# Optimization experiments

Hardware: AMD Instinct MI355X
Metric: run time of the kernel (lower is better)

Reference implementation:

```python
import jax, jax.numpy as jnp
import numpy as np

DN = ('NCHW', 'OIHW', 'NCHW')
HEADS = 4
EPS_LN = 1e-5
EPS_NORM = 1e-12


def conv(x, w, pad=0, groups=1):
    return jax.lax.conv_general_dilated(
        x, w, window_strides=(1, 1), padding=[(pad, pad), (pad, pad)],
        dimension_numbers=DN, feature_group_count=groups)


def layernorm(x, w, b):
    # LayerNorm over channel axis per spatial position (to_3d -> LN(c) -> to_4d)
    mu = jnp.mean(x, axis=1, keepdims=True)
    var = jnp.mean((x - mu) ** 2, axis=1, keepdims=True)
    return (x - mu) / jnp.sqrt(var + EPS_LN) * w[None, :, None, None] + b[None, :, None, None]


def setup_inputs() -> dict:
    key = jax.random.key(0)
    ks = jax.random.split(key, 12)
    b, dim, h, w = 2, 192, 128, 128
    hidden = int(dim * 2.66)  # 510

    def rn(k, shape, scale=0.05):
        return jax.random.normal(k, shape, dtype=jnp.float32) * scale

    return {
        'x': jax.random.normal(ks[0], (b, dim, h, w), dtype=jnp.float32),
        'illum': jax.random.normal(ks[1], (b, dim, h, w), dtype=jnp.float32),
        'ln1_w': jnp.ones((dim,), jnp.float32), 'ln1_b': jnp.zeros((dim,), jnp.float32),
        'lnL_w': jnp.ones((dim,), jnp.float32), 'lnL_b': jnp.zeros((dim,), jnp.float32),
        'ln2_w': jnp.ones((dim,), jnp.float32), 'ln2_b': jnp.zeros((dim,), jnp.float32),
        'q_w': rn(ks[2], (dim, dim, 1, 1)),
        'qdw_w': rn(ks[3], (dim, dim, 3, 3)),        # full 3x3 conv (no groups in source)
        'kv_w': rn(ks[4], (2 * dim, dim, 1, 1)),
        'kvdw_w': rn(ks[5], (2 * dim, 1, 3, 3)),     # depthwise, groups = 2*dim
        'temp': jnp.ones((HEADS, 1, 1), jnp.float32),
        'proj_w': rn(ks[6], (dim, dim, 1, 1)),
        'pin_w': rn(ks[7], (hidden, dim, 1, 1)),
        'dw_w': rn(ks[8], (hidden, hidden, 3, 3)),   # full 3x3 conv (no groups in source)
        'pout_w': rn(ks[9], (dim, hidden, 1, 1)),
    }


def _block(x, illum, ln1_w, ln1_b, lnL_w, lnL_b, ln2_w, ln2_b,
           q_w, qdw_w, kv_w, kvdw_w, temp, proj_w, pin_w, dw_w, pout_w):
    b, c, h, w = x.shape
    ch = c // HEADS

    # ---- Illum-guided channel attention (MDTA) ----
    xn = layernorm(x, ln1_w, ln1_b)
    iln = layernorm(illum, lnL_w, lnL_b)
    q = conv(conv(iln, q_w), qdw_w, pad=1)
    kv = conv(conv(xn, kv_w), kvdw_w, pad=1, groups=2 * c)
    k, v = jnp.split(kv, 2, axis=1)

    def split_heads(t):
        return t.reshape(b, HEADS, ch, h * w)  # b head c (hw)

    q, k, v = split_heads(q), split_heads(k), split_heads(v)
    q = q / jnp.maximum(jnp.linalg.norm(q, axis=-1, keepdims=True), EPS_NORM)
    k = k / jnp.maximum(jnp.linalg.norm(k, axis=-1, keepdims=True), EPS_NORM)

    attn = jnp.einsum('bhce,bhde->bhcd', q, k) * temp[None]  # [b, head, ch, ch]
    attn = jax.nn.softmax(attn, axis=-1)
    out = jnp.einsum('bhcd,bhde->bhce', attn, v).reshape(b, c, h, w)
    x = x + conv(out, proj_w)

    # ---- FFN: 1x1 -> full 3x3 -> GELU -> 1x1 ----
    xn2 = layernorm(x, ln2_w, ln2_b)
    f = conv(xn2, pin_w)
    f = jax.nn.gelu(conv(f, dw_w, pad=1), approximate=False)
    x = x + conv(f, pout_w)
    return x


def reference(x, illum, ln1_w, ln1_b, lnL_w, lnL_b, ln2_w, ln2_b,
              q_w, qdw_w, kv_w, kvdw_w, temp, proj_w, pin_w, dw_w, pout_w):
    return _block(x, illum, ln1_w, ln1_b, lnL_w, lnL_b, ln2_w, ln2_b,
                  q_w, qdw_w, kv_w, kvdw_w, temp, proj_w, pin_w, dw_w, pout_w)
```

## Files before the change

### kernel.cpp

```cpp
#include <hip/hip_runtime.h>
#include <hip/hip_bf16.h>

typedef __hip_bfloat16 bf16;
typedef __attribute__((ext_vector_type(8))) short bf16x8v;
typedef __attribute__((ext_vector_type(4))) float f32x4;

namespace {
constexpr int B_  = 2;
constexpr int C_  = 192;
constexpr int HW_ = 128 * 128;
constexpr int C2_ = 384;
}

static __device__ __forceinline__ float fb(bf16 v) { return __bfloat162float(v); }
static __device__ __forceinline__ bf16 tob(float v) { return __float2bfloat16(v); }

typedef __attribute__((address_space(1))) const char GChar;
typedef __attribute__((address_space(3))) char LChar;
static __device__ __forceinline__ void gl16(const void* g, void* l) {
    __builtin_amdgcn_global_load_lds((GChar*)g, (LChar*)l, 16, 0, 0);
}
static __device__ __forceinline__ bf16x8v lread(const bf16* base, int row, int slot) {
    const char* p = (const char*)base + (size_t)row * 128 + ((size_t)((slot ^ (row & 7))) << 4);
    return *(const bf16x8v*)p;
}

static __device__ __forceinline__ void rp1(const float* W, bf16* Wr, int blk, int t,
                                           int N, int K, int Npad, int Kpad) {
    int i = blk * 256 + t;
    if (i >= Npad * Kpad) return;
    int n = i / Kpad, k = i % Kpad;
    float v = (n < N && k < K) ? W[n * K + k] : 0.f;
    Wr[i] = tob(v);
}
static __device__ __forceinline__ void rp3(const float* W, bf16* Wr, int blk, int t,
                                           int N, int K, int Npad, int Kpad) {
    int i = blk * 256 + t;
    int NK = Npad * Kpad;
    if (i >= NK) return;
    int n = i / Kpad, k = i % Kpad;
    if (n < N && k < K) {
        const float* src = W + ((size_t)(n * K + k)) * 9;
#pragma unroll
        for (int q = 0; q < 9; q++) Wr[(size_t)q * NK + i] = tob(src[q]);
    } else {
#pragma unroll
        for (int q = 0; q < 9; q++) Wr[(size_t)q * NK + i] = tob(0.f);
    }
}

__global__ __launch_bounds__(256) void k_repack_ln(
    const float* __restrict__ qw, const float* __restrict__ kvw,
    const float* __restrict__ projw, const float* __restrict__ pinw,
    const float* __restrict__ poutw, const float* __restrict__ qdww,
    const float* __restrict__ dww,
    bf16* __restrict__ Wq1, bf16* __restrict__ Wkv, bf16* __restrict__ Wproj,
    bf16* __restrict__ Wpin, bf16* __restrict__ Wpout, bf16* __restrict__ Wqdw,
    bf16* __restrict__ Wdw, char* __restrict__ zpage,
    const float* __restrict__ X0, const float* __restrict__ X1,
    const float* __restrict__ w0, const float* __restrict__ b0,
    const float* __restrict__ w1, const float* __restrict__ b1,
    bf16* __restrict__ out0, bf16* __restrict__ out1) {
    __shared__ float lds[64][C_ + 1];
    int blk = blockIdx.x, t = threadIdx.x;
    if (blk < 144)        { rp1(qw,    Wq1,   blk,        t, 192, 192, 192, 192); return; }
    else if (blk < 432)   { rp1(kvw,   Wkv,   blk - 144,  t, 384, 192, 384, 192); return; }
    else if (blk < 576)   { rp1(projw, Wproj, blk - 432,  t, 192, 192, 192, 192); return; }
    else if (blk < 960)   { rp1(pinw,  Wpin,  blk - 576,  t, 510, 192, 512, 192); return; }
    else if (blk < 1344)  { rp1(poutw, Wpout, blk - 960,  t, 192, 510, 192, 512); return; }
    else if (blk < 1488)  { rp3(qdww,  Wqdw,  blk - 1344, t, 192, 192, 192, 192); return; }
    else if (blk < 2512)  { rp3(dww,   Wdw,   blk - 1488, t, 510, 510, 512, 512); return; }
    else if (blk == 2512) { ((uint4*)zpage)[t] = make_uint4(0u, 0u, 0u, 0u); return; }
    int lb = blk - 2513;
    int sel = lb >> 9, xb = lb & 511;
    const float* X = sel ? X1 : X0;
    const float* w = sel ? w1 : w0;
    const float* bb = sel ? b1 : b0;
    bf16* out = sel ? out1 : out0;
    int p0 = xb * 64;
    int b = p0 / HW_, pi0 = p0 % HW_;
    for (int i = t; i < 64 * C_ / 4; i += 256) {
        int c = i >> 4, pp4 = (i & 15) << 2;
        float4 v = *(const float4*)(X + ((size_t)(b * C_ + c)) * HW_ + pi0 + pp4);
        lds[pp4 + 0][c] = v.x; lds[pp4 + 1][c] = v.y;
        lds[pp4 + 2][c] = v.z; lds[pp4 + 3][c] = v.w;
    }
    __syncthreads();
    int pp = t >> 2, qq = t & 3;
    float s = 0.f, s2 = 0.f;
    for (int c = qq * 48; c < qq * 48 + 48; c++) { float v = lds[pp][c]; s += v; s2 += v * v; }
    s  += __shfl_xor(s, 1);  s  += __shfl_xor(s, 2);
    s2 += __shfl_xor(s2, 1); s2 += __shfl_xor(s2, 2);
    float mu = s / C_;
    float rstd = rsqrtf(s2 / C_ - mu * mu + 1e-5f);
    bf16* ob = out + ((size_t)(p0 + pp)) * C_ + qq * 48;
#pragma unroll
    for (int j = 0; j < 6; j++) {
        union { bf16 h[8]; uint4 u; } ov;
#pragma unroll
        for (int e = 0; e < 8; e++) {
            int c = qq * 48 + j * 8 + e;
            ov.h[e] = tob((lds[pp][c] - mu) * rstd * w[c] + bb[c]);
        }
        *(uint4*)(ob + j * 8) = ov.u;
    }
}

__global__ __launch_bounds__(256) void k_ln_pc(const bf16* __restrict__ X2,
                                               const float* __restrict__ w,
                                               const float* __restrict__ bb,
                                               bf16* __restrict__ out) {
    int t = threadIdx.x;
    int p = blockIdx.x * 64 + (t >> 2), qq = t & 3;
    const bf16* row = X2 + (size_t)p * C_ + qq * 48;
    uint4 u[6];
#pragma unroll
    for (int j = 0; j < 6; j++) u[j] = *(const uint4*)(row + j * 8);
    float s = 0.f, s2 = 0.f;
#pragma unroll
    for (int j = 0; j < 6; j++) {
        const bf16* pv = (const bf16*)&u[j];
#pragma unroll
        for (int e = 0; e < 8; e++) { float v = fb(pv[e]); s += v; s2 += v * v; }
    }
    s  += __shfl_xor(s, 1);  s  += __shfl_xor(s, 2);
    s2 += __shfl_xor(s2, 1); s2 += __shfl_xor(s2, 2);
    float mu = s / C_;
    float rstd = rsqrtf(s2 / C_ - mu * mu + 1e-5f);
    bf16* orow = out + (size_t)p * C_ + qq * 48;
#pragma unroll
    for (int j = 0; j < 6; j++) {
        const bf16* pv = (const bf16*)&u[j];
        union { bf16 h[8]; uint4 u4; } ov;
#pragma unroll
        for (int e = 0; e < 8; e++) {
            int c = qq * 48 + j * 8 + e;
            ov.h[e] = tob((fb(pv[e]) - mu) * rstd * w[c] + bb[c]);
        }
        *(uint4*)(orow + j * 8) = ov.u4;
    }
}

template <int BN, int EPI>
static __device__ __forceinline__ void gemm1x1_body(const bf16* __restrict__ A,
                                                    const bf16* __restrict__ Wbase,
                                                    const int K, const int Cout,
                                                    void* __restrict__ outp,
                                                    const void* __restrict__ resid,
                                                    const int mt, const int n0) {
    constexpr int WN = BN / 2, FN = WN / 16, BIT = BN / 32;
    __shared__ __align__(16) bf16 As[128 * 64];
    __shared__ __align__(16) bf16 Bs[BN * 64];
    const int t = threadIdx.x;
    const int b = mt >> 7, y = mt & 127;
    const int w = t >> 6, lane = t & 63;
    const int wm = w >> 1, wn = w & 1;
    const int g = lane >> 4, r = lane & 15;
    const int ldw = t - lane;

    f32x4 acc[4][FN];
#pragma unroll
    for (int i = 0; i < 4; i++)
#pragma unroll
        for (int j = 0; j < FN; j++) acc[i][j] = {0.f, 0.f, 0.f, 0.f};

    const bf16* Abase = A + (size_t)mt * 128 * K;

    for (int c0 = 0; c0 < K; c0 += 64) {
#pragma unroll
        for (int it = 0; it < 4; it++) {
            int idx = it * 256 + t;
            int row = idx >> 3, sl = idx & 7;
            const char* gp = (const char*)(Abase + (size_t)row * K + c0) + ((sl ^ (row & 7)) << 4);
            gl16(gp, (char*)As + (size_t)(it * 256 + ldw) * 16);
        }
#pragma unroll
        for (int it = 0; it < BIT; it++) {
            int idx = it * 256 + t;
            int row = idx >> 3, sl = idx & 7;
            const char* gp = (const char*)(Wbase + (size_t)(n0 + row) * K + c0) + ((sl ^ (row & 7)) << 4);
            gl16(gp, (char*)Bs + (size_t)(it * 256 + ldw) * 16);
        }
        __syncthreads();
#pragma unroll
        for (int ks = 0; ks < 2; ks++) {
            bf16x8v af[4], bv[FN];
#pragma unroll
            for (int fm = 0; fm < 4; fm++)
                af[fm] = lread(As, wm * 64 + fm * 16 + r, ks * 4 + g);
#pragma unroll
            for (int fn = 0; fn < FN; fn++)
                bv[fn] = lread(Bs, wn * WN + fn * 16 + r, ks * 4 + g);
#pragma unroll
            for (int fm = 0; fm < 4; fm++)
#pragma unroll
                for (int fn = 0; fn < FN; fn++)
                    acc[fm][fn] = __builtin_amdgcn_mfma_f32_16x16x32_bf16(af[fm], bv[fn], acc[fm][fn], 0, 0, 0);
        }
        __syncthreads();
    }

#pragma unroll
    for (int fm = 0; fm < 4; fm++)
#pragma unroll
        for (int fn = 0; fn < FN; fn++)
#pragma unroll
            for (int reg = 0; reg < 4; reg++) {
                int xl = wm * 64 + fm * 16 + g * 4 + reg;
                int co = n0 + wn * WN + fn * 16 + r;
                float v = acc[fm][fn][reg];
                if constexpr (EPI == 1) {
                    ((bf16*)outp)[((size_t)mt * 128 + xl) * Cout + co] = tob(v);
                } else if constexpr (EPI == 2) {
                    v += ((const float*)resid)[((size_t)(b * C_ + co)) * HW_ + y * 128 + xl];
                    ((bf16*)outp)[((size_t)mt * 128 + xl) * C_ + co] = tob(v);
                } else {
                    v += fb(((const bf16*)resid)[((size_t)mt * 128 + xl) * C_ + co]);
                    ((float*)outp)[((size_t)(b * C_ + co)) * HW_ + y * 128 + xl] = v;
                }
            }
}

template <int BN, int EPI>
__global__ __launch_bounds__(256) void k_gemm1x1(const bf16* __restrict__ A,
                                                 const bf16* __restrict__ Wr,
                                                 const int K, const int Cout,
                                                 void* __restrict__ outp,
                                                 const void* __restrict__ resid,
                                                 const int wbstride) {
    const int mt = blockIdx.x;
    const bf16* Wbase = Wr + (size_t)(mt >> 7) * wbstride;
    gemm1x1_body<BN, EPI>(A, Wbase, K, Cout, outp, resid, mt, blockIdx.y * BN);
}

__global__ __launch_bounds__(256) void k_qkv(const bf16* __restrict__ iln,
                                             const bf16* __restrict__ xn,
                                             const bf16* __restrict__ Wq1,
                                             const bf16* __restrict__ Wkv,
                                             bf16* __restrict__ qtmp,
                                             bf16* __restrict__ kvtmp) {
    const bool isq = blockIdx.y < 2;
    const bf16* A = isq ? iln : xn;
    const bf16* Wr = isq ? Wq1 : Wkv;
    bf16* outp = isq ? qtmp : kvtmp;
    const int Cout = isq ? 192 : 384;
    const int n0 = (isq ? blockIdx.y : blockIdx.y - 2) * 96;
    gemm1x1_body<96, 1>(A, Wr, 192, Cout, outp, nullptr, blockIdx.x, n0);
}

template <int BN, int EPI>
__global__ __launch_bounds__(256) void k_gemm3x3(const bf16* __restrict__ A,
                                                 const bf16* __restrict__ Wr,
                                                 const int Cin, const int Cout,
                                                 bf16* __restrict__ outp,
                                                 const char* __restrict__ zpage) {
    constexpr int WN = BN / 2, FN = WN / 16, BIT = BN / 32;
    __shared__ __align__(16) bf16 As[160 * 64];
    __shared__ __align__(16) bf16 Bs[BN * 64];
    const int t = threadIdx.x;
    const int mtRaw = blockIdx.x;
    const int mt = ((mtRaw & 7) << 5) | (mtRaw >> 3);
    const int n0 = blockIdx.y * BN;
    const int b = mt >> 7, y = mt & 127;
    const int w = t >> 6, lane = t & 63;
    const int wm = w >> 1, wn = w & 1;
    const int g = lane >> 4, r = lane & 15;
    const int ldw = t - lane;

    f32x4 acc[4][FN];
#pragma unroll
    for (int i = 0; i < 4; i++)
#pragma unroll
        for (int j = 0; j < FN; j++) acc[i][j] = {0.f, 0.f, 0.f, 0.f};

    for (int ky = 0; ky < 3; ky++) {
        const int yy = y + ky - 1;
        if (yy < 0 || yy > 127) continue;
        const bf16* Ab = A + ((size_t)b * HW_ + (size_t)yy * 128) * Cin;
        for (int c0 = 0; c0 < Cin; c0 += 64) {
            for (int kx = 0; kx < 3; kx++) {
                if (kx == 0) {
#pragma unroll
                    for (int it = 0; it < 5; it++) {
                        int idx = it * 256 + t;
                        int row = idx >> 3, sl = idx & 7;
                        int so = (sl ^ (row & 7)) << 4;
                        const char* gp = (row >= 1 && row <= 128)
                            ? (const char*)(Ab + (size_t)(row - 1) * Cin + c0) + so
                            : zpage + so;
                        gl16(gp, (char*)As + (size_t)(it * 256 + ldw) * 16);
                    }
                }
                const bf16* Wb = Wr + (size_t)(ky * 3 + kx) * Cout * Cin;
#pragma unroll
                for (int it = 0; it < BIT; it++) {
                    int idx = it * 256 + t;
                    int row = idx >> 3, sl = idx & 7;
                    const char* gp = (const char*)(Wb + (size_t)(n0 + row) * Cin + c0) + ((sl ^ (row & 7)) << 4);
                    gl16(gp, (char*)Bs + (size_t)(it * 256 + ldw) * 16);
                }
                __syncthreads();
#pragma unroll
                for (int ks = 0; ks < 2; ks++) {
                    bf16x8v af[4], bv[FN];
#pragma unroll
                    for (int fm = 0; fm < 4; fm++)
                        af[fm] = lread(As, wm * 64 + fm * 16 + r + kx, ks * 4 + g);
#pragma unroll
                    for (int fn = 0; fn < FN; fn++)
                        bv[fn] = lread(Bs, wn * WN + fn * 16 + r, ks * 4 + g);
#pragma unroll
                    for (int fm = 0; fm < 4; fm++)
#pragma unroll
                        for (int fn = 0; fn < FN; fn++)
                            acc[fm][fn] = __builtin_amdgcn_mfma_f32_16x16x32_bf16(af[fm], bv[fn], acc[fm][fn], 0, 0, 0);
                }
                __syncthreads();
            }
        }
    }
#pragma unroll
    for (int fm = 0; fm < 4; fm++)
#pragma unroll
        for (int fn = 0; fn < FN; fn++)
#pragma unroll
            for (int reg = 0; reg < 4; reg++) {
                int xl = wm * 64 + fm * 16 + g * 4 + reg;
                int co = n0 + wn * WN + fn * 16 + r;
                float v = acc[fm][fn][reg];
                if constexpr (EPI == 1) v = 0.5f * v * (1.0f + erff(v * 0.70710678118654752f));
                outp[((size_t)mt * 128 + xl) * Cout + co] = tob(v);
            }
}

__global__ __launch_bounds__(192) void k_dwconv2(const bf16* __restrict__ kv,
                                                 const float* __restrict__ wdw,
                                                 bf16* __restrict__ kout,
                                                 bf16* __restrict__ vout) {
    __shared__ float wlds[1728];
    const int t = threadIdx.x;
    const int row = blockIdx.x;
    const int z = blockIdx.y;
    const int b = row >> 7, y = row & 127;
    for (int i = t; i < 432; i += 192)
        ((float4*)wlds)[i] = ((const float4*)(wdw + (size_t)z * 1728))[i];
    __syncthreads();
    const int c8h = t % 24, xg = t / 24;
    const int cbase = z * C_ + c8h * 8;
    float wreg[9][8];
#pragma unroll
    for (int tap = 0; tap < 9; tap++)
#pragma unroll
        for (int j = 0; j < 8; j++) wreg[tap][j] = wlds[(c8h * 8 + j) * 9 + tap];

    bf16* outb = (z == 0 ? kout : vout) + (size_t)(b * HW_ + y * 128) * C_ + c8h * 8;
    const uint4 zero4 = make_uint4(0u, 0u, 0u, 0u);
    const int x0 = xg * 16;
    bool vy[3]; const bf16* rowp[3];
#pragma unroll
    for (int ky = 0; ky < 3; ky++) {
        int yy = y + ky - 1;
        vy[ky] = (yy >= 0 && yy <= 127);
        int yyc = vy[ky] ? yy : 0;
        rowp[ky] = kv + ((size_t)b * HW_ + (size_t)yyc * 128) * C2_ + cbase;
    }
    uint4 win[3][3];
#pragma unroll
    for (int ky = 0; ky < 3; ky++) {
        win[ky][0] = (vy[ky] && x0 - 1 >= 0) ? *(const uint4*)(rowp[ky] + (size_t)(x0 - 1) * C2_) : zero4;
        win[ky][1] = vy[ky] ? *(const uint4*)(rowp[ky] + (size_t)x0 * C2_) : zero4;
    }
    for (int i = 0; i < 16; i++) {
        int x = x0 + i;
#pragma unroll
        for (int ky = 0; ky < 3; ky++)
            win[ky][2] = (vy[ky] && x + 1 <= 127) ? *(const uint4*)(rowp[ky] + (size_t)(x + 1) * C2_) : zero4;
        float acc[8];
#pragma unroll
        for (int j = 0; j < 8; j++) acc[j] = 0.f;
#pragma unroll
        for (int ky = 0; ky < 3; ky++)
#pragma unroll
            for (int kx = 0; kx < 3; kx++) {
                const bf16* pv = (const bf16*)&win[ky][kx];
#pragma unroll
                for (int j = 0; j < 8; j++)
                    acc[j] += fb(pv[j]) * wreg[ky * 3 + kx][j];
            }
        union { bf16 h[8]; uint4 u; } ov;
#pragma unroll
        for (int j = 0; j < 8; j++) ov.h[j] = tob(acc[j]);
        *(uint4*)(outb + (size_t)x * C_) = ov.u;
#pragma unroll
        for (int ky = 0; ky < 3; ky++) { win[ky][0] = win[ky][1]; win[ky][1] = win[ky][2]; }
    }
}

__global__ __launch_bounds__(256) void k_qk(const bf16* __restrict__ q,
                                            const bf16* __restrict__ k,
                                            float* __restrict__ Spart,
                                            float* __restrict__ ssq) {
    __shared__ float qs[64][49];
    __shared__ float ks[64][49];
    __shared__ float redq[4][48], redk[4][48];
    int t = threadIdx.x;
    int ch = blockIdx.x, hd = blockIdx.y, b = blockIdx.z;
    int i0 = (t >> 4) * 3, j0 = (t & 15) * 3;
    int cs = t % 48, qr = t / 48;
    float acc[3][3];
    float sq = 0.f, sk = 0.f;
#pragma unroll
    for (int a = 0; a < 3; a++)
#pragma unroll
        for (int c = 0; c < 3; c++) acc[a][c] = 0.f;

    for (int sub = 0; sub < 4; sub++) {
        size_t rbase = ((size_t)b * HW_ + ch * 256 + sub * 64) * C_ + hd * 48;
        for (int i = t; i < 64 * 6; i += 256) {
            int row = i / 6, oc = i % 6;
            uint4 v = *(const uint4*)(q + rbase + (size_t)row * C_ + oc * 8);
            const bf16* pv = (const bf16*)&v;
#pragma unroll
            for (int j = 0; j < 8; j++) qs[row][oc * 8 + j] = fb(pv[j]);
            uint4 v2 = *(const uint4*)(k + rbase + (size_t)row * C_ + oc * 8);
            const bf16* pv2 = (const bf16*)&v2;
#pragma unroll
            for (int j = 0; j < 8; j++) ks[row][oc * 8 + j] = fb(pv2[j]);
        }
        __syncthreads();
        if (t < 192) {
#pragma unroll
            for (int rr = 0; rr < 16; rr++) {
                float qv = qs[qr * 16 + rr][cs]; sq += qv * qv;
                float kv2 = ks[qr * 16 + rr][cs]; sk += kv2 * kv2;
            }
        }
        for (int p = 0; p < 64; p++) {
            float a0 = qs[p][i0], a1 = qs[p][i0 + 1], a2 = qs[p][i0 + 2];
            float b0 = ks[p][j0], b1 = ks[p][j0 + 1], b2 = ks[p][j0 + 2];
            acc[0][0] += a0 * b0; acc[0][1] += a0 * b1; acc[0][2] += a0 * b2;
            acc[1][0] += a1 * b0; acc[1][1] += a1 * b1; acc[1][2] += a1 * b2;
            acc[2][0] += a2 * b0; acc[2][1] += a2 * b1; acc[2][2] += a2 * b2;
        }
        __syncthreads();
    }
    if (t < 192) { redq[qr][cs] = sq; redk[qr][cs] = sk; }
    float* dst = Spart + (((size_t)(b * 4 + hd)) * 64 + ch) * 2304;
#pragma unroll
    for (int a = 0; a < 3; a++)
#pragma unroll
        for (int c = 0; c < 3; c++) dst[(i0 + a) * 48 + (j0 + c)] = acc[a][c];
    __syncthreads();
    if (t < 48) {
        float s0 = redq[0][t] + redq[1][t] + redq[2][t] + redq[3][t];
        float s1 = redk[0][t] + redk[1][t] + redk[2][t] + redk[3][t];
        ssq[((size_t)b * 64 + ch) * C_ + hd * 48 + t] = s0;
        ssq[((size_t)(2 + b) * 64 + ch) * C_ + hd * 48 + t] = s1;
    }
}

__global__ __launch_bounds__(256) void k_softmax(const float* __restrict__ Spart,
                                                 const float* __restrict__ ssq,
                                                 const float* __restrict__ temp,
                                                 bf16* __restrict__ attnW) {
    __shared__ float S[2304];
    __shared__ float invk_s[48];
    int t = threadIdx.x;
    int hd = blockIdx.x, b = blockIdx.y;
    const float* base = Spart + ((size_t)(b * 4 + hd)) * 64 * 2304;
    for (int e = t; e < 2304; e += 256) {
        float s = 0.f;
        for (int ch = 0; ch < 64; ch++) s += base[(size_t)ch * 2304 + e];
        S[e] = s;
    }
    if (t < 48) {
        int c = hd * 48 + t;
        float sk = 0.f;
        for (int ch = 0; ch < 64; ch++) sk += ssq[((size_t)(2 + b) * 64 + ch) * C_ + c];
        invk_s[t] = 1.f / fmaxf(sqrtf(sk), 1e-12f);
    }
    __syncthreads();
    if (t >= 48) return;
    int c = hd * 48 + t;
    float sq = 0.f;
    for (int ch = 0; ch < 64; ch++) sq += ssq[((size_t)b * 64 + ch) * C_ + c];
    float qi = 1.f / fmaxf(sqrtf(sq), 1e-12f);
    float tp = temp[hd];
    float row[48];
    float mx = -1e30f;
    for (int j = 0; j < 48; j++) {
        float s = S[t * 48 + j] * qi * invk_s[j] * tp;
        row[j] = s;
        mx = fmaxf(mx, s);
    }
    float sum = 0.f;
    for (int j = 0; j < 48; j++) { row[j] = expf(row[j] - mx); sum += row[j]; }
    float is = 1.f / sum;
    bf16* wrow = attnW + ((size_t)b * 192 + hd * 48 + t) * 192 + hd * 48;
    for (int j = 0; j < 48; j++) wrow[j] = tob(row[j] * is);
}

__global__ __launch_bounds__(256) void k_wav(const bf16* __restrict__ Wproj,
                                             const bf16* __restrict__ attnW,
                                             bf16* __restrict__ Mw) {
    int bid = blockIdx.x;
    int b = bid / 12, rg = bid % 12;
    int t = threadIdx.x;
    int row = rg * 16 + (t >> 4);
    int c0b = (t & 15) * 12;
    int hd = c0b / 48;
    const bf16* aw = attnW + (size_t)b * 36864;
    float acc[12];
#pragma unroll
    for (int j = 0; j < 12; j++) acc[j] = 0.f;
    for (int k = hd * 48; k < hd * 48 + 48; k++) {
        float wp = fb(Wproj[row * 192 + k]);
        const bf16* ar = aw + (size_t)k * 192 + c0b;
#pragma unroll
        for (int j = 0; j < 12; j++) acc[j] += wp * fb(ar[j]);
    }
    bf16* mrow = Mw + ((size_t)b * 192 + row) * 192 + c0b;
#pragma unroll
    for (int j = 0; j < 12; j++) mrow[j] = tob(acc[j]);
}

extern "C" void kernel_launch(void* const* d_in, const int* in_sizes, int n_in,
                              void* d_out, int out_size, void* d_ws, size_t ws_size,
                              hipStream_t stream) {
    const float* x     = (const float*)d_in[0];
    const float* illum = (const float*)d_in[1];
    const float* ln1w  = (const float*)d_in[2];
    const float* ln1b  = (const float*)d_in[3];
    const float* lnLw  = (const float*)d_in[4];
    const float* lnLb  = (const float*)d_in[5];
    const float* ln2w  = (const float*)d_in[6];
    const float* ln2b  = (const float*)d_in[7];
    const float* qw    = (const float*)d_in[8];
    const float* qdww  = (const float*)d_in[9];
    const float* kvw   = (const float*)d_in[10];
    const float* kvdww = (const float*)d_in[11];
    const float* temp  = (const float*)d_in[12];
    const float* projw = (const float*)d_in[13];
    const float* pinw  = (const float*)d_in[14];
    const float* dww   = (const float*)d_in[15];
    const float* poutw = (const float*)d_in[16];

    char* ws = (char*)d_ws;
    bf16*  Wq1   = (bf16*)(ws + 0);
    bf16*  Wkv   = (bf16*)(ws + 73728);
    bf16*  Wqdw  = (bf16*)(ws + 221184);
    bf16*  Wproj = (bf16*)(ws + 884736);
    bf16*  Wpin  = (bf16*)(ws + 958464);
    bf16*  Wdw   = (bf16*)(ws + 1155072);
    bf16*  Wpout = (bf16*)(ws + 5873664);
    float* ssq   = (float*)(ws + 6070272);
    char*  zpage = (char*)(ws + 6266880);
    const size_t A0 = 6270976, u = 12582912;
    bf16* xn    = (bf16*)(ws + A0 + 0 * u);
    bf16* iln   = (bf16*)(ws + A0 + 1 * u);
    bf16* qtmp  = (bf16*)(ws + A0 + 2 * u);
    bf16* qb    = (bf16*)(ws + A0 + 1 * u);
    bf16* kvtmp = (bf16*)(ws + A0 + 2 * u);
    bf16* vb    = (bf16*)(ws + A0 + 4 * u);
    float* Spart = (float*)(ws + A0 + 3 * u);
    bf16*  attnW = (bf16*)(ws + A0 + 3 * u + 4718592);
    bf16*  Mw    = (bf16*)(ws + A0 + 3 * u + 4866048);
    bf16* kb    = (bf16*)(ws + A0 + 0 * u);
    bf16* x2    = (bf16*)(ws + A0 + 0 * u);
    bf16* xn2   = (bf16*)(ws + A0 + 3 * u);
    bf16* fbuf  = (bf16*)(ws + A0 + 4 * u);
    bf16* gbuf  = (bf16*)(ws + A0 + 1 * u);
    qtmp  = (bf16*)(ws + A0 + 4 * u);
    kvtmp = (bf16*)(ws + A0 + 2 * u);
    qb    = (bf16*)(ws + A0 + 1 * u);
    vb    = (bf16*)(ws + A0 + 4 * u + 12582912);

    k_repack_ln<<<3537, 256, 0, stream>>>(qw, kvw, projw, pinw, poutw, qdww, dww,
                                          Wq1, Wkv, Wproj, Wpin, Wpout, Wqdw, Wdw, zpage,
                                          x, illum, ln1w, ln1b, lnLw, lnLb, xn, iln);

    k_qkv<<<dim3(256, 6), 256, 0, stream>>>(iln, xn, Wq1, Wkv, qtmp, kvtmp);

    k_gemm3x3<96, 0><<<dim3(256, 2), 256, 0, stream>>>(qtmp, Wqdw, 192, 192, qb, zpage);
    k_dwconv2<<<dim3(256, 2), 192, 0, stream>>>(kvtmp, kvdww, kb, vb);

    k_qk<<<dim3(64, 4, 2), 256, 0, stream>>>(qb, kb, Spart, ssq);
    k_softmax<<<dim3(4, 2), 256, 0, stream>>>(Spart, ssq, temp, attnW);
    k_wav<<<24, 256, 0, stream>>>(Wproj, attnW, Mw);

    k_gemm1x1<96, 2><<<dim3(256, 2), 256, 0, stream>>>(vb, Mw, 192, 192, x2, x, 36864);

    k_ln_pc<<<512, 256, 0, stream>>>(x2, ln2w, ln2b, xn2);
    k_gemm1x1<128, 1><<<dim3(256, 4), 256, 0, stream>>>(xn2, Wpin, 192, 512, fbuf, nullptr, 0);
    k_gemm3x3<128, 1><<<dim3(256, 4), 256, 0, stream>>>(fbuf, Wdw, 512, 512, gbuf, zpage);
    k_gemm1x1<96, 3><<<dim3(256, 2), 256, 0, stream>>>(gbuf, Wpout, 512, 192, d_out, x2, 0);
}
```

Baseline: 371.8 us.

## Replace FFN 3x3 conv GEMM with two-row tile kernel reusing A across kx taps

Adds a dedicated kernel for the 512->512 full 3x3 FFN conv. Each 512-thread block covers two image rows (256 pixels) by 128 output channels and loads a haloed 130-pixel strip per input row once per channel chunk, then reuses it for all three kx taps by shifting the LDS row index. This cuts redundant A-tile global loads and doubles the M tile. It also swizzles the block index order for locality. Workspace pointer declarations are tidied with identical final addresses. The cost is larger LDS use (about 56 KB), possibly lower occupancy, and a sync per tap with no double buffering.

```diff
diff --git a/kernel.cpp b/kernel.cpp
--- a/kernel.cpp
+++ b/kernel.cpp
@@ -333,6 +333,93 @@
             }
 }
 
+__global__ __launch_bounds__(512) void k_dw3x3b(const bf16* __restrict__ A,
+                                                const bf16* __restrict__ Wr,
+                                                bf16* __restrict__ outp,
+                                                const char* __restrict__ zpage) {
+    constexpr int CI = 512, CO = 512;
+    __shared__ __align__(16) bf16 As[320 * 64];
+    __shared__ __align__(16) bf16 Bs[128 * 64];
+    const int t = threadIdx.x;
+    const int mtRaw = blockIdx.x;
+    const int mt = ((mtRaw & 7) << 4) | (mtRaw >> 3);
+    const int n0 = blockIdx.y * 128;
+    const int b = mt >> 6, y0 = mt & 63;
+    const int w = t >> 6, lane = t & 63;
+    const int wm = w >> 1, wn = w & 1;
+    const int g = lane >> 4, r = lane & 15;
+
+    f32x4 acc[4][4];
+#pragma unroll
+    for (int i = 0; i < 4; i++)
+#pragma unroll
+        for (int j = 0; j < 4; j++) acc[i][j] = {0.f, 0.f, 0.f, 0.f};
+
+    for (int ky = 0; ky < 3; ky++) {
+        for (int c0 = 0; c0 < CI; c0 += 64) {
+            for (int kx = 0; kx < 3; kx++) {
+                if (kx == 0) {
+#pragma unroll
+                    for (int it = 0; it < 5; it++) {
+                        int idx = it * 512 + t;
+                        int row = idx >> 3, sl = idx & 7;
+                        int so = (sl ^ (row & 7)) << 4;
+                        int rr = (row >= 160) ? 1 : 0;
+                        int xr = row - rr * 160;
+                        int ya = 2 * y0 + ky - 1 + rr;
+                        bool valid = (xr >= 1 && xr <= 128 && ya >= 0 && ya <= 127);
+                        const char* gp = valid
+                            ? (const char*)(A + ((size_t)(b * HW_ + ya * 128 + xr - 1)) * CI + c0) + so
+                            : zpage + so;
+                        gl16(gp, (char*)As + (size_t)(it * 512 + (t - lane)) * 16);
+                    }
+                }
+                const bf16* Wb = Wr + (size_t)(ky * 3 + kx) * CO * CI + c0;
+#pragma unroll
+                for (int it = 0; it < 2; it++) {
+                    int idx = it * 512 + t;
+                    int row = idx >> 3, sl = idx & 7;
+                    const char* gp = (const char*)(Wb + (size_t)(n0 + row) * CI) + ((sl ^ (row & 7)) << 4);
+                    gl16(gp, (char*)Bs + (size_t)(it * 512 + (t - lane)) * 16);
+                }
+                __syncthreads();
+#pragma unroll
+                for (int ks = 0; ks < 2; ks++) {
+                    bf16x8v af[4], bv[4];
+#pragma unroll
+                    for (int fm = 0; fm < 4; fm++) {
+                        int p = wm * 64 + fm * 16 + r;
+                        int rowA = ((p >> 7) * 160) + (p & 127) + kx;
+                        af[fm] = lread(As, rowA, ks * 4 + g);
+                    }
+#pragma unroll
+                    for (int fn = 0; fn < 4; fn++)
+                        bv[fn] = lread(Bs, wn * 64 + fn * 16 + r, ks * 4 + g);
+#pragma unroll
+                    for (int fm = 0; fm < 4; fm++)
+#pragma unroll
+                        for (int fn = 0; fn < 4; fn++)
+                            acc[fm][fn] = __builtin_amdgcn_mfma_f32_16x16x32_bf16(af[fm], bv[fn], acc[fm][fn], 0, 0, 0);
+                }
+                __syncthreads();
+            }
+        }
+    }
+#pragma unroll
+    for (int fm = 0; fm < 4; fm++)
+#pragma unroll
+        for (int fn = 0; fn < 4; fn++)
+#pragma unroll
+            for (int reg = 0; reg < 4; reg++) {
+                int p = wm * 64 + fm * 16 + g * 4 + reg;
+                int yloc = p >> 7, xx = p & 127;
+                int co = n0 + wn * 64 + fn * 16 + r;
+                float v = acc[fm][fn][reg];
+                v = 0.5f * v * (1.0f + erff(v * 0.70710678118654752f));
+                outp[((size_t)(b * HW_ + (2 * y0 + yloc) * 128 + xx)) * CO + co] = tob(v);
+            }
+}
+
 __global__ __launch_bounds__(192) void k_dwconv2(const bf16* __restrict__ kv,
                                                  const float* __restrict__ wdw,
                                                  bf16* __restrict__ kout,
@@ -558,22 +645,18 @@
     const size_t A0 = 6270976, u = 12582912;
     bf16* xn    = (bf16*)(ws + A0 + 0 * u);
     bf16* iln   = (bf16*)(ws + A0 + 1 * u);
-    bf16* qtmp  = (bf16*)(ws + A0 + 2 * u);
+    bf16* kvtmp = (bf16*)(ws + A0 + 2 * u);
+    bf16* qtmp  = (bf16*)(ws + A0 + 4 * u);
     bf16* qb    = (bf16*)(ws + A0 + 1 * u);
-    bf16* kvtmp = (bf16*)(ws + A0 + 2 * u);
-    bf16* vb    = (bf16*)(ws + A0 + 4 * u);
+    bf16* kb    = (bf16*)(ws + A0 + 0 * u);
+    bf16* vb    = (bf16*)(ws + A0 + 4 * u + 12582912);
     float* Spart = (float*)(ws + A0 + 3 * u);
     bf16*  attnW = (bf16*)(ws + A0 + 3 * u + 4718592);
     bf16*  Mw    = (bf16*)(ws + A0 + 3 * u + 4866048);
-    bf16* kb    = (bf16*)(ws + A0 + 0 * u);
     bf16* x2    = (bf16*)(ws + A0 + 0 * u);
     bf16* xn2   = (bf16*)(ws + A0 + 3 * u);
     bf16* fbuf  = (bf16*)(ws + A0 + 4 * u);
     bf16* gbuf  = (bf16*)(ws + A0 + 1 * u);
-    qtmp  = (bf16*)(ws + A0 + 4 * u);
-    kvtmp = (bf16*)(ws + A0 + 2 * u);
-    qb    = (bf16*)(ws + A0 + 1 * u);
-    vb    = (bf16*)(ws + A0 + 4 * u + 12582912);
 
     k_repack_ln<<<3537, 256, 0, stream>>>(qw, kvw, projw, pinw, poutw, qdww, dww,
                                           Wq1, Wkv, Wproj, Wpin, Wpout, Wqdw, Wdw, zpage,
@@ -592,6 +675,6 @@
 
     k_ln_pc<<<512, 256, 0, stream>>>(x2, ln2w, ln2b, xn2);
     k_gemm1x1<128, 1><<<dim3(256, 4), 256, 0, stream>>>(xn2, Wpin, 192, 512, fbuf, nullptr, 0);
-    k_gemm3x3<128, 1><<<dim3(256, 4), 256, 0, stream>>>(fbuf, Wdw, 512, 512, gbuf, zpage);
+    k_dw3x3b<<<dim3(128, 4), 512, 0, stream>>>(fbuf, Wdw, gbuf, zpage);
     k_gemm1x1<96, 3><<<dim3(256, 2), 256, 0, stream>>>(gbuf, Wpout, 512, 192, d_out, x2, 0);
 }
```

Result: slower. 389.6 us (+4.8%).
